# Kernel optimization log

Measured on AMD Instinct MI355X. Metric: run time of the kernel, lower is better.

The kernel has to match this reference:

```python
import jax, jax.numpy as jnp
import numpy as np

N = 262144       # batch rows
C = 256          # in_channels
K = 256          # uint8 code range


def setup_inputs() -> dict:
    key = jax.random.key(0)
    k1, k2, k3, k4 = jax.random.split(key, 4)
    left = jax.random.randint(k1, (N, C), 0, K, dtype=jnp.int32)
    right = jax.random.randint(k2, (N, C), 0, K, dtype=jnp.int32)
    # per-channel 256x256 lookup tables: white_table[c][l, r] -> new code in [0, 256)
    white_table = jax.random.randint(k3, (C, K, K), 0, K, dtype=jnp.int32)
    # per-channel last-layer codebook: last_codebook[c][1][code] -> float
    codebook = jax.random.normal(k4, (C, K), dtype=jnp.float32)
    return {"left": left, "right": right, "white_table": white_table, "codebook": codebook}


def reference(left, right, white_table, codebook):
    # Fused equivalent of the per-channel python loop:
    #   for c: codes[:, c] = white_table[c][left[:, c], right[:, c]]
    #   out[:, c]  = codebook[c][codes[:, c]]
    ch = jnp.arange(C, dtype=jnp.int32)[None, :]          # [1, C] broadcasts vs [N, C]
    codes = white_table[ch, left, right]                   # [N, C] int32 gather
    out = codebook[ch, codes]                              # [N, C] float32 gather
    return out
```

## Files before the change

### kernel.cpp

```cpp
#include <hip/hip_runtime.h>
#include <hip/hip_bf16.h>
#include <stdint.h>

#define CCH   256
#define KK    256
#define ROWS_PER_BLOCK 512

__global__ __launch_bounds__(256) void compress_table_kernel(
    const int4* __restrict__ t, uchar4* __restrict__ o, int n4) {
  int i = blockIdx.x * 256 + threadIdx.x;
  if (i < n4) {
    int4 v = t[i];
    o[i] = make_uchar4((unsigned char)v.x, (unsigned char)v.y,
                       (unsigned char)v.z, (unsigned char)v.w);
  }
}

template <typename TabT>
__global__ __launch_bounds__(256) void gather_kernel(
    const int4* __restrict__ left, const int4* __restrict__ right,
    const TabT* __restrict__ tab, const float* __restrict__ cb,
    float4* __restrict__ out, int nrows) {
  __shared__ float cbs[32 * KK];

  const int g     = blockIdx.x & 7;
  const int chunk = blockIdx.x >> 3;
  const int q     = threadIdx.x & 7;
  const int rsub  = threadIdx.x >> 3;

  {
    const float4* cbg = (const float4*)(cb + (size_t)(g * 32) * KK);
    float4* cbl = (float4*)cbs;
#pragma unroll
    for (int i = 0; i < 8; ++i) cbl[threadIdx.x + i * 256] = cbg[threadIdx.x + i * 256];
  }
  __syncthreads();

  const int cbase = g * 32 + q * 4;
  const TabT* t0 = tab + (size_t)cbase * (KK * KK);
  const int vecoff = g * 8 + q;

  int row = chunk * ROWS_PER_BLOCK + rsub;
#pragma unroll 4
  for (int it = 0; it < ROWS_PER_BLOCK / 32; ++it, row += 32) {
    if (row >= nrows) break;
    size_t vi = (size_t)row * 64 + vecoff;
    int4 L = left[vi];
    int4 R = right[vi];

    unsigned c0 = (unsigned)t0[          (unsigned)(L.x * KK + R.x)];
    unsigned c1 = (unsigned)t0[ 65536u + (unsigned)(L.y * KK + R.y)];
    unsigned c2 = (unsigned)t0[131072u + (unsigned)(L.z * KK + R.z)];
    unsigned c3 = (unsigned)t0[196608u + (unsigned)(L.w * KK + R.w)];

    float4 o;
    o.x = cbs[(q * 4 + 0) * KK + c0];
    o.y = cbs[(q * 4 + 1) * KK + c1];
    o.z = cbs[(q * 4 + 2) * KK + c2];
    o.w = cbs[(q * 4 + 3) * KK + c3];
    out[vi] = o;
  }
}

extern "C" void kernel_launch(void* const* d_in, const int* in_sizes, int n_in,
                              void* d_out, int out_size, void* d_ws, size_t ws_size,
                              hipStream_t stream) {
  const int*   left  = (const int*)d_in[0];
  const int*   right = (const int*)d_in[1];
  const int*   wt    = (const int*)d_in[2];
  const float* cb    = (const float*)d_in[3];
  float* out = (float*)d_out;

  const int nrows = in_sizes[0] / CCH;
  const int tab_elems = CCH * KK * KK;
  const int blocks = ((nrows + ROWS_PER_BLOCK - 1) / ROWS_PER_BLOCK) * 8;

  if (ws_size >= (size_t)tab_elems) {
    unsigned char* tab8 = (unsigned char*)d_ws;
    int n4 = tab_elems / 4;
    compress_table_kernel<<<n4 / 256, 256, 0, stream>>>(
        (const int4*)wt, (uchar4*)tab8, n4);
    gather_kernel<unsigned char><<<blocks, 256, 0, stream>>>(
        (const int4*)left, (const int4*)right, tab8, cb, (float4*)out, nrows);
  } else {
    gather_kernel<int><<<blocks, 256, 0, stream>>>(
        (const int4*)left, (const int4*)right, wt, cb, (float4*)out, nrows);
  }
}
```

Measured before the change: 877.3 us.

## Split channels into 16 groups, process two rows per thread, use nontemporal streams

Each block now covers 16 channels instead of 32, which halves the codebook held in shared memory (16 KB) and adds an occupancy hint of 8 blocks per SM through launch bounds. Each thread handles two rows per iteration so more independent table gathers are in flight at once. The left/right loads and the output stores use nontemporal builtins so the streamed data does not push the table out of cache. The cost is twice as many blocks, which doubles the shared-memory codebook fills, and somewhat more register pressure.

```diff
diff --git a/kernel.cpp b/kernel.cpp
--- a/kernel.cpp
+++ b/kernel.cpp
@@ -1,10 +1,14 @@
 #include <hip/hip_runtime.h>
-#include <hip/hip_bf16.h>
 #include <stdint.h>
 
 #define CCH   256
 #define KK    256
 #define ROWS_PER_BLOCK 512
+#define NGROUPS 16
+#define GCH   (CCH / NGROUPS)
+
+typedef int   i32x4 __attribute__((ext_vector_type(4)));
+typedef float f32x4 __attribute__((ext_vector_type(4)));
 
 __global__ __launch_bounds__(256) void compress_table_kernel(
     const int4* __restrict__ t, uchar4* __restrict__ o, int n4) {
@@ -17,48 +21,79 @@
 }
 
 template <typename TabT>
-__global__ __launch_bounds__(256) void gather_kernel(
-    const int4* __restrict__ left, const int4* __restrict__ right,
+__global__ __launch_bounds__(256, 8) void gather_kernel(
+    const i32x4* __restrict__ left, const i32x4* __restrict__ right,
     const TabT* __restrict__ tab, const float* __restrict__ cb,
-    float4* __restrict__ out, int nrows) {
-  __shared__ float cbs[32 * KK];
+    f32x4* __restrict__ out, int nrows) {
+  __shared__ float cbs[GCH * KK];
 
-  const int g     = blockIdx.x & 7;
-  const int chunk = blockIdx.x >> 3;
-  const int q     = threadIdx.x & 7;
-  const int rsub  = threadIdx.x >> 3;
+  const int g     = blockIdx.x & (NGROUPS - 1);
+  const int chunk = blockIdx.x / NGROUPS;
+  const int q     = threadIdx.x & 3;
+  const int rsub  = threadIdx.x >> 2;
 
   {
-    const float4* cbg = (const float4*)(cb + (size_t)(g * 32) * KK);
-    float4* cbl = (float4*)cbs;
+    const f32x4* cbg = (const f32x4*)(cb + (size_t)(g * GCH) * KK);
+    f32x4* cbl = (f32x4*)cbs;
 #pragma unroll
-    for (int i = 0; i < 8; ++i) cbl[threadIdx.x + i * 256] = cbg[threadIdx.x + i * 256];
+    for (int i = 0; i < 4; ++i) cbl[threadIdx.x + i * 256] = cbg[threadIdx.x + i * 256];
   }
   __syncthreads();
 
-  const int cbase = g * 32 + q * 4;
-  const TabT* t0 = tab + (size_t)cbase * (KK * KK);
-  const int vecoff = g * 8 + q;
+  const int cbase  = g * GCH + q * 4;
+  const TabT* t0   = tab + (size_t)cbase * (KK * KK);
+  const int vecoff = g * 4 + q;
+  const float* cq  = cbs + (q * 4) * KK;
 
-  int row = chunk * ROWS_PER_BLOCK + rsub;
-#pragma unroll 4
-  for (int it = 0; it < ROWS_PER_BLOCK / 32; ++it, row += 32) {
-    if (row >= nrows) break;
-    size_t vi = (size_t)row * 64 + vecoff;
-    int4 L = left[vi];
-    int4 R = right[vi];
+  const int rbase = chunk * ROWS_PER_BLOCK;
+#pragma unroll
+  for (int it = 0; it < ROWS_PER_BLOCK / 128; ++it) {
+    const int r0 = rbase + it * 128 + rsub;
+    if (r0 >= nrows) break;
+    const int r1 = r0 + 64;
+    const unsigned v0 = (unsigned)r0 * 64u + (unsigned)vecoff;
+    const unsigned v1 = (unsigned)r1 * 64u + (unsigned)vecoff;
 
-    unsigned c0 = (unsigned)t0[          (unsigned)(L.x * KK + R.x)];
-    unsigned c1 = (unsigned)t0[ 65536u + (unsigned)(L.y * KK + R.y)];
-    unsigned c2 = (unsigned)t0[131072u + (unsigned)(L.z * KK + R.z)];
-    unsigned c3 = (unsigned)t0[196608u + (unsigned)(L.w * KK + R.w)];
+    if (r1 < nrows) {
+      i32x4 L0 = __builtin_nontemporal_load(&left[v0]);
+      i32x4 R0 = __builtin_nontemporal_load(&right[v0]);
+      i32x4 L1 = __builtin_nontemporal_load(&left[v1]);
+      i32x4 R1 = __builtin_nontemporal_load(&right[v1]);
 
-    float4 o;
-    o.x = cbs[(q * 4 + 0) * KK + c0];
-    o.y = cbs[(q * 4 + 1) * KK + c1];
-    o.z = cbs[(q * 4 + 2) * KK + c2];
-    o.w = cbs[(q * 4 + 3) * KK + c3];
-    out[vi] = o;
+      unsigned c00 = (unsigned)t0[          (unsigned)(L0[0] * KK + R0[0])];
+      unsigned c01 = (unsigned)t0[ 65536u + (unsigned)(L0[1] * KK + R0[1])];
+      unsigned c02 = (unsigned)t0[131072u + (unsigned)(L0[2] * KK + R0[2])];
+      unsigned c03 = (unsigned)t0[196608u + (unsigned)(L0[3] * KK + R0[3])];
+      unsigned c10 = (unsigned)t0[          (unsigned)(L1[0] * KK + R1[0])];
+      unsigned c11 = (unsigned)t0[ 65536u + (unsigned)(L1[1] * KK + R1[1])];
+      unsigned c12 = (unsigned)t0[131072u + (unsigned)(L1[2] * KK + R1[2])];
+      unsigned c13 = (unsigned)t0[196608u + (unsigned)(L1[3] * KK + R1[3])];
+
+      f32x4 o0, o1;
+      o0[0] = cq[         c00];
+      o0[1] = cq[  KK   + c01];
+      o0[2] = cq[2*KK   + c02];
+      o0[3] = cq[3*KK   + c03];
+      o1[0] = cq[         c10];
+      o1[1] = cq[  KK   + c11];
+      o1[2] = cq[2*KK   + c12];
+      o1[3] = cq[3*KK   + c13];
+      __builtin_nontemporal_store(o0, &out[v0]);
+      __builtin_nontemporal_store(o1, &out[v1]);
+    } else {
+      i32x4 L0 = __builtin_nontemporal_load(&left[v0]);
+      i32x4 R0 = __builtin_nontemporal_load(&right[v0]);
+      unsigned c00 = (unsigned)t0[          (unsigned)(L0[0] * KK + R0[0])];
+      unsigned c01 = (unsigned)t0[ 65536u + (unsigned)(L0[1] * KK + R0[1])];
+      unsigned c02 = (unsigned)t0[131072u + (unsigned)(L0[2] * KK + R0[2])];
+      unsigned c03 = (unsigned)t0[196608u + (unsigned)(L0[3] * KK + R0[3])];
+      f32x4 o0;
+      o0[0] = cq[         c00];
+      o0[1] = cq[  KK   + c01];
+      o0[2] = cq[2*KK   + c02];
+      o0[3] = cq[3*KK   + c03];
+      __builtin_nontemporal_store(o0, &out[v0]);
+    }
   }
 }
 
@@ -73,7 +108,8 @@
 
   const int nrows = in_sizes[0] / CCH;
   const int tab_elems = CCH * KK * KK;
-  const int blocks = ((nrows + ROWS_PER_BLOCK - 1) / ROWS_PER_BLOCK) * 8;
+  const int chunks = (nrows + ROWS_PER_BLOCK - 1) / ROWS_PER_BLOCK;
+  const int blocks = chunks * NGROUPS;
 
   if (ws_size >= (size_t)tab_elems) {
     unsigned char* tab8 = (unsigned char*)d_ws;
@@ -81,9 +117,9 @@
     compress_table_kernel<<<n4 / 256, 256, 0, stream>>>(
         (const int4*)wt, (uchar4*)tab8, n4);
     gather_kernel<unsigned char><<<blocks, 256, 0, stream>>>(
-        (const int4*)left, (const int4*)right, tab8, cb, (float4*)out, nrows);
+        (const i32x4*)left, (const i32x4*)right, tab8, cb, (f32x4*)out, nrows);
   } else {
     gather_kernel<int><<<blocks, 256, 0, stream>>>(
-        (const int4*)left, (const int4*)right, wt, cb, (float4*)out, nrows);
+        (const i32x4*)left, (const i32x4*)right, wt, cb, (f32x4*)out, nrows);
   }
 }
```

Result: slower. 900.5 us (+2.6%).
